# Performance work log

Measured on AMD Instinct MI355X. Metric: run time of the kernel, lower is better.

The kernel has to match this reference:

```python
import jax, jax.numpy as jnp
import numpy as np

B = 4          # documents per batch
L = 128        # unique candidate entity links
S = 2048       # predicted spans (max over batch)
N = 1 + L + S  # root + links + spans


def setup_inputs() -> dict:
    key = jax.random.key(0)
    k1, k2, k3 = jax.random.split(key, 3)
    # coref/linking edge scores over [root | links | spans] x [root | links | spans]
    scores = jax.random.normal(k1, (B, N, N), dtype=jnp.float32) * 0.1
    eye = jnp.eye(N, dtype=jnp.float32)
    # z mask: all admissible edges -- no self loops, no incoming edges to root
    z_mask = jnp.ones((B, N, N), dtype=jnp.float32) * (1.0 - eye)[None]
    z_mask = z_mask.at[:, :, 0].set(0.0)
    # target mask: sparse subset of z edges + root->all so a spanning
    # arborescence always exists (mirrors the gold cluster / gold link edges)
    tgt = (jax.random.uniform(k2, (B, N, N)) < 0.05).astype(jnp.float32) * z_mask
    tgt = tgt.at[:, 0, 1:].set(1.0)
    # ragged valid lengths per batch element (1 + unique_links_len + n_pred_spans)
    lengths = jnp.array([N, N - 256, N - 512, N - 64], dtype=jnp.int32)
    return {"scores": scores, "target_mask": tgt, "z_mask": z_mask, "lengths": lengths}


def _mtt_log_partition(scores, mask, lengths):
    """Matrix-tree theorem log-partition: logdet of the root-minor of the
    Laplacian of exp(scores) restricted to edges in `mask` and to the first
    `lengths[b]` nodes of each batch element."""
    n = scores.shape[-1]
    valid = (jnp.arange(n)[None, :] < lengths[:, None]).astype(scores.dtype)  # [B,N]
    w = jnp.exp(scores) * mask * valid[:, :, None] * valid[:, None, :]        # [B,N,N]
    colsum = jnp.sum(w, axis=-2)                                              # incoming weight per node
    lap = colsum[:, :, None] * jnp.eye(n, dtype=scores.dtype)[None] - w       # L = D_in - W
    minor = lap[:, 1:, 1:]                                                    # drop root row/col
    # pad the diagonal of invalid (past-length) nodes with 1 so they
    # contribute logdet 0 instead of making the minor singular
    pad = 1.0 - valid[:, 1:]
    minor = minor + pad[:, :, None] * jnp.eye(n - 1, dtype=scores.dtype)[None]
    _, logdet = jnp.linalg.slogdet(minor)
    return logdet


def reference(scores, target_mask, z_mask, lengths):
    log_z = _mtt_log_partition(scores, z_mask, lengths)        # log partition over all arborescences
    log_t = _mtt_log_partition(scores, target_mask, lengths)   # log weight of gold arborescences
    return jnp.mean(log_z - log_t)                             # MTT negative log-likelihood
```

## Files before the change

### kernel.cpp

```cpp
#include <hip/hip_runtime.h>
#include <math.h>

#define NFULL 2177
#define NN    2176
#define NB    64
#define NMAT  8
#define NBATCH 4


__global__ void init_cs_kernel(float* __restrict__ cs) {
  int i = blockIdx.x * blockDim.x + threadIdx.x;
  if (i < NMAT * NN) cs[i] = 0.f;
}

__global__ __launch_bounds__(256) void build_fused(const float* __restrict__ scores,
                                                   const float* __restrict__ zm,
                                                   const float* __restrict__ tm,
                                                   const int* __restrict__ lengths,
                                                   float* __restrict__ cs,
                                                   float* __restrict__ M) {
  int c = blockIdx.x * 256 + threadIdx.x;
  if (c >= NN) return;
  int b = blockIdx.z;
  int len = lengths[b];
  int j = c + 1;
  bool jv = (j < len);
  int r0 = blockIdx.y * 64;
  size_t sbase = (size_t)b * NFULL * NFULL + j;
  float az = 0.f, at = 0.f;
  if (blockIdx.y == 0 && jv) {
    float e = __expf(scores[sbase]);
    az += e * zm[sbase];
    at += e * tm[sbase];
  }
  size_t mz = (size_t)b * NN * NN + (size_t)r0 * NN + c;
  size_t mt = (size_t)(NBATCH + b) * NN * NN + (size_t)r0 * NN + c;
  for (int rr = 0; rr < 64; ++rr) {
    int i = r0 + rr + 1;
    float vz = 0.f, vt = 0.f;
    if (jv && i < len) {
      size_t off = sbase + (size_t)i * NFULL;
      float e = __expf(scores[off]);
      vz = e * zm[off];
      vt = e * tm[off];
      az += vz;
      at += vt;
    }
    M[mz] = -vz;
    M[mt] = -vt;
    mz += NN;
    mt += NN;
  }
  if (az != 0.f) atomicAdd(&cs[b * NN + c], az);
  if (at != 0.f) atomicAdd(&cs[(NBATCH + b) * NN + c], at);
}

__global__ void diag_fix(const int* __restrict__ lengths,
                         const float* __restrict__ cs,
                         float* __restrict__ M) {
  int idx = blockIdx.x * 256 + threadIdx.x;
  if (idx >= NMAT * NN) return;
  int mm = idx / NN, c = idx - mm * NN;
  int len = lengths[mm & 3];
  float pad = (c + 1 < len) ? 0.f : 1.f;
  M[(size_t)mm * NN * NN + (size_t)c * NN + c] = cs[idx] + pad;
}


__device__ void factor_invert(float* __restrict__ A,
                              float* __restrict__ invUg,
                              float* __restrict__ invLg,
                              float (*T)[68], float (*X)[68],
                              float* __restrict__ Dinv,
                              int k0, int tid, int do_inv) {
  for (int j = 0; j < 63; ++j) {
    float inv = 1.0f / T[j][j];
    for (int r = j + 1 + tid; r < 64; r += 256) T[r][j] *= inv;
    __syncthreads();
    int rem = 63 - j;
    for (int idx = tid; idx < rem * rem; idx += 256) {
      int rr = j + 1 + idx / rem;
      int cc = j + 1 + idx % rem;
      T[rr][cc] -= T[rr][j] * T[j][cc];
    }
    __syncthreads();
  }
  for (int idx = tid; idx < 64 * 64; idx += 256) {
    int r = idx >> 6, c = idx & 63;
    A[(size_t)(k0 + r) * NN + (k0 + c)] = T[r][c];
  }
  if (!do_inv) return;
  if (tid < 64) Dinv[tid] = 1.0f / T[tid][tid];
  __syncthreads();
  if (tid < 64) {
    int j = tid;
    X[j][j] = Dinv[j];
    for (int i = j - 1; i >= 0; --i) {
      float s = 0.f;
      for (int t = i + 1; t <= j; ++t) s += T[i][t] * X[t][j];
      X[i][j] = -s * Dinv[i];
    }
    for (int i = j + 1; i < 64; ++i) X[i][j] = 0.f;
  }
  __syncthreads();
  for (int idx = tid; idx < 4096; idx += 256) invUg[idx] = X[idx >> 6][idx & 63];
  __syncthreads();
  if (tid < 64) {
    int j = tid;
    X[j][j] = 1.f;
    for (int i = j + 1; i < 64; ++i) {
      float s = 0.f;
      for (int t = j; t < i; ++t) s += T[i][t] * X[t][j];
      X[i][j] = -s;
    }
    for (int i = 0; i < j; ++i) X[i][j] = 0.f;
  }
  __syncthreads();
  for (int idx = tid; idx < 4096; idx += 256) invLg[idx] = X[idx >> 6][idx & 63];
}

__global__ __launch_bounds__(256) void factor0(float* __restrict__ Mb,
                                               float* __restrict__ invUb,
                                               float* __restrict__ invLb) {
  __shared__ float T[64][68];
  __shared__ float X[64][68];
  __shared__ float Dinv[64];
  int m = blockIdx.x, tid = threadIdx.x;
  float* A = Mb + (size_t)m * NN * NN;
  for (int idx = tid; idx < 64 * 64; idx += 256) {
    int r = idx >> 6, c = idx & 63;
    T[r][c] = A[(size_t)r * NN + c];
  }
  __syncthreads();
  factor_invert(A, invUb + (size_t)m * 4096, invLb + (size_t)m * 4096,
                T, X, Dinv, 0, tid, 1);
}

__global__ __launch_bounds__(256) void panel_gemm(float* __restrict__ Mb,
                                                  const float* __restrict__ invUb,
                                                  const float* __restrict__ invLb,
                                                  int k0) {
  __shared__ float Aa[64][68];
  __shared__ float Bb[64][68];
  int m = blockIdx.y, role = blockIdx.z, tid = threadIdx.x;
  float* A = Mb + (size_t)m * NN * NN;
  int obase = k0 + 64 + blockIdx.x * 64;
  if (role == 0) {
    const float* invU = invUb + (size_t)m * 4096;
    for (int idx = tid; idx < 4096; idx += 256) {
      int r = idx >> 6, k = idx & 63;
      Aa[k][r] = A[(size_t)(obase + r) * NN + (k0 + k)];
    }
    for (int idx = tid; idx < 4096; idx += 256)
      Bb[idx >> 6][idx & 63] = invU[idx];
  } else {
    const float* invL = invLb + (size_t)m * 4096;
    for (int idx = tid; idx < 4096; idx += 256) {
      int r = idx >> 6, k = idx & 63;
      Aa[k][r] = invL[(r << 6) + k];
    }
    for (int idx = tid; idx < 4096; idx += 256) {
      int k = idx >> 6, c = idx & 63;
      Bb[k][c] = A[(size_t)(k0 + k) * NN + (obase + c)];
    }
  }
  __syncthreads();
  int c0 = (tid & 15) << 2;
  int r0 = (tid >> 4) << 2;
  float acc[4][4];
#pragma unroll
  for (int i = 0; i < 4; ++i)
#pragma unroll
    for (int jj = 0; jj < 4; ++jj) acc[i][jj] = 0.f;
#pragma unroll 8
  for (int k = 0; k < 64; ++k) {
    float4 a  = *(const float4*)&Aa[k][r0];
    float4 bv = *(const float4*)&Bb[k][c0];
    acc[0][0] += a.x * bv.x; acc[0][1] += a.x * bv.y; acc[0][2] += a.x * bv.z; acc[0][3] += a.x * bv.w;
    acc[1][0] += a.y * bv.x; acc[1][1] += a.y * bv.y; acc[1][2] += a.y * bv.z; acc[1][3] += a.y * bv.w;
    acc[2][0] += a.z * bv.x; acc[2][1] += a.z * bv.y; acc[2][2] += a.z * bv.z; acc[2][3] += a.z * bv.w;
    acc[3][0] += a.w * bv.x; acc[3][1] += a.w * bv.y; acc[3][2] += a.w * bv.z; acc[3][3] += a.w * bv.w;
  }
  if (role == 0) {
#pragma unroll
    for (int i = 0; i < 4; ++i) {
      float4 v = make_float4(acc[i][0], acc[i][1], acc[i][2], acc[i][3]);
      *(float4*)&A[(size_t)(obase + r0 + i) * NN + (k0 + c0)] = v;
    }
  } else {
#pragma unroll
    for (int i = 0; i < 4; ++i) {
      float4 v = make_float4(acc[i][0], acc[i][1], acc[i][2], acc[i][3]);
      *(float4*)&A[(size_t)(k0 + r0 + i) * NN + (obase + c0)] = v;
    }
  }
}

__global__ __launch_bounds__(256) void trail_gemm(float* __restrict__ Mb,
                                                  float* __restrict__ invUb,
                                                  float* __restrict__ invLb,
                                                  int k0, int do_inv) {
  __shared__ float Lt[64][68];
  __shared__ float Ut[64][68];
  __shared__ float Dinv[64];
  int m = blockIdx.z;
  float* A = Mb + (size_t)m * NN * NN;
  int base  = k0 + 64;
  int rbase = base + blockIdx.y * 64;
  int cbase = base + blockIdx.x * 64;
  int tid = threadIdx.x;
  for (int idx = tid; idx < 64 * 64; idx += 256) {
    int r = idx >> 6, k = idx & 63;
    Lt[k][r] = A[(size_t)(rbase + r) * NN + (k0 + k)];
  }
  for (int idx = tid; idx < 64 * 64; idx += 256) {
    int k = idx >> 6, c = idx & 63;
    Ut[k][c] = A[(size_t)(k0 + k) * NN + (cbase + c)];
  }
  __syncthreads();
  int c0 = (tid & 15) << 2;
  int r0 = (tid >> 4) << 2;
  float acc[4][4];
#pragma unroll
  for (int i = 0; i < 4; ++i)
#pragma unroll
    for (int jj = 0; jj < 4; ++jj) acc[i][jj] = 0.f;
#pragma unroll 8
  for (int k = 0; k < 64; ++k) {
    float4 a  = *(const float4*)&Lt[k][r0];
    float4 bv = *(const float4*)&Ut[k][c0];
    acc[0][0] += a.x * bv.x; acc[0][1] += a.x * bv.y; acc[0][2] += a.x * bv.z; acc[0][3] += a.x * bv.w;
    acc[1][0] += a.y * bv.x; acc[1][1] += a.y * bv.y; acc[1][2] += a.y * bv.z; acc[1][3] += a.y * bv.w;
    acc[2][0] += a.z * bv.x; acc[2][1] += a.z * bv.y; acc[2][2] += a.z * bv.z; acc[2][3] += a.z * bv.w;
    acc[3][0] += a.w * bv.x; acc[3][1] += a.w * bv.y; acc[3][2] += a.w * bv.z; acc[3][3] += a.w * bv.w;
  }
  bool special = (blockIdx.x == 0 && blockIdx.y == 0);
  if (!special) {
#pragma unroll
    for (int i = 0; i < 4; ++i) {
      float4* p = (float4*)&A[(size_t)(rbase + r0 + i) * NN + (cbase + c0)];
      float4 v = *p;
      v.x -= acc[i][0]; v.y -= acc[i][1]; v.z -= acc[i][2]; v.w -= acc[i][3];
      *p = v;
    }
    return;
  }
  __syncthreads();
#pragma unroll
  for (int i = 0; i < 4; ++i) {
    const float4* p = (const float4*)&A[(size_t)(rbase + r0 + i) * NN + (cbase + c0)];
    float4 v = *p;
    v.x -= acc[i][0]; v.y -= acc[i][1]; v.z -= acc[i][2]; v.w -= acc[i][3];
    *(float4*)&Lt[r0 + i][c0] = v;
  }
  __syncthreads();
  factor_invert(A, invUb + (size_t)m * 4096, invLb + (size_t)m * 4096,
                Lt, Ut, Dinv, base, tid, do_inv);
}


__global__ void logdet_kernel(const float* __restrict__ Mb, double* __restrict__ dlog) {
  int m = blockIdx.x;
  const float* A = Mb + (size_t)m * NN * NN;
  double s = 0.0;
  for (int i = threadIdx.x; i < NN; i += 256)
    s += (double)logf(fabsf(A[(size_t)i * NN + i]));
  __shared__ double red[256];
  red[threadIdx.x] = s;
  __syncthreads();
  for (int k = 128; k > 0; k >>= 1) {
    if (threadIdx.x < k) red[threadIdx.x] += red[threadIdx.x + k];
    __syncthreads();
  }
  if (threadIdx.x == 0) dlog[m] = red[0];
}

__global__ void final_kernel(const double* __restrict__ dlog, float* __restrict__ out) {
  if (threadIdx.x == 0) {
    double acc = 0.0;
    for (int b = 0; b < NBATCH; ++b) acc += dlog[b] - dlog[NBATCH + b];
    out[0] = (float)(acc * 0.25);
  }
}


extern "C" void kernel_launch(void* const* d_in, const int* in_sizes, int n_in,
                              void* d_out, int out_size, void* d_ws, size_t ws_size,
                              hipStream_t stream) {
  const float* scores  = (const float*)d_in[0];
  const float* tm      = (const float*)d_in[1];
  const float* zm      = (const float*)d_in[2];
  const int*   lengths = (const int*)d_in[3];
  float* out = (float*)d_out;

  float* M  = (float*)d_ws;
  float* cs = M + (size_t)NMAT * NN * NN;
  double* dlog = (double*)(cs + (size_t)NMAT * NN);
  float* invU = (float*)(dlog + NMAT);
  float* invL = invU + (size_t)NMAT * 4096;

  init_cs_kernel<<<(NMAT * NN + 255) / 256, 256, 0, stream>>>(cs);
  build_fused<<<dim3((NN + 255) / 256, NN / 64, NBATCH), 256, 0, stream>>>(
      scores, zm, tm, lengths, cs, M);
  diag_fix<<<(NMAT * NN + 255) / 256, 256, 0, stream>>>(lengths, cs, M);
  factor0<<<NMAT, 256, 0, stream>>>(M, invU, invL);

  for (int k0 = 0; k0 + NB < NN; k0 += NB) {
    int rem = NN - k0 - NB;
    panel_gemm<<<dim3(rem / 64, NMAT, 2), 256, 0, stream>>>(M, invU, invL, k0);
    trail_gemm<<<dim3(rem / 64, rem / 64, NMAT), 256, 0, stream>>>(
        M, invU, invL, k0, rem > 64 ? 1 : 0);
  }

  logdet_kernel<<<NMAT, 256, 0, stream>>>(M, dlog);
  final_kernel<<<1, 64, 0, stream>>>(dlog, out);
}
```

Measured before the change: 5.321 ms.

## Use 128x128 trailing-update tiles and restructure diagonal block factorization

Result: slower. 5.774 ms (+8.5%).

```diff
diff --git a/kernel.cpp b/kernel.cpp
--- a/kernel.cpp
+++ b/kernel.cpp
@@ -6,6 +6,10 @@
 #define NB    64
 #define NMAT  8
 #define NBATCH 4
+#define TP    65
+#define LTP   132
+#define UTP   140
+#define SSZ   8704
 
 
 __global__ void init_cs_kernel(float* __restrict__ cs) {
@@ -67,73 +71,55 @@
 }
 
 
-__device__ void factor_invert(float* __restrict__ A,
-                              float* __restrict__ invUg,
-                              float* __restrict__ invLg,
-                              float (*T)[68], float (*X)[68],
-                              float* __restrict__ Dinv,
-                              int k0, int tid, int do_inv) {
+__device__ __forceinline__ void factor64(float* T, int tid) {
+  int c = tid & 63, g = tid >> 6;
   for (int j = 0; j < 63; ++j) {
-    float inv = 1.0f / T[j][j];
-    for (int r = j + 1 + tid; r < 64; r += 256) T[r][j] *= inv;
+    float inv = 1.0f / T[j * TP + j];
+    int rs = j + 1 + ((g - j - 1) & 3);
+    if (c == j) {
+      for (int r = rs; r < 64; r += 4) T[r * TP + j] *= inv;
+    }
     __syncthreads();
-    int rem = 63 - j;
-    for (int idx = tid; idx < rem * rem; idx += 256) {
-      int rr = j + 1 + idx / rem;
-      int cc = j + 1 + idx % rem;
-      T[rr][cc] -= T[rr][j] * T[j][cc];
+    if (c > j) {
+      float ujc = T[j * TP + c];
+      for (int r = rs; r < 64; r += 4) T[r * TP + c] -= T[r * TP + j] * ujc;
     }
     __syncthreads();
   }
-  for (int idx = tid; idx < 64 * 64; idx += 256) {
-    int r = idx >> 6, c = idx & 63;
-    A[(size_t)(k0 + r) * NN + (k0 + c)] = T[r][c];
-  }
-  if (!do_inv) return;
-  if (tid < 64) Dinv[tid] = 1.0f / T[tid][tid];
-  __syncthreads();
-  if (tid < 64) {
-    int j = tid;
-    X[j][j] = Dinv[j];
-    for (int i = j - 1; i >= 0; --i) {
-      float s = 0.f;
-      for (int t = i + 1; t <= j; ++t) s += T[i][t] * X[t][j];
-      X[i][j] = -s * Dinv[i];
-    }
-    for (int i = j + 1; i < 64; ++i) X[i][j] = 0.f;
-  }
-  __syncthreads();
-  for (int idx = tid; idx < 4096; idx += 256) invUg[idx] = X[idx >> 6][idx & 63];
-  __syncthreads();
-  if (tid < 64) {
-    int j = tid;
-    X[j][j] = 1.f;
-    for (int i = j + 1; i < 64; ++i) {
-      float s = 0.f;
-      for (int t = j; t < i; ++t) s += T[i][t] * X[t][j];
-      X[i][j] = -s;
-    }
-    for (int i = 0; i < j; ++i) X[i][j] = 0.f;
-  }
-  __syncthreads();
-  for (int idx = tid; idx < 4096; idx += 256) invLg[idx] = X[idx >> 6][idx & 63];
-}
-
-__global__ __launch_bounds__(256) void factor0(float* __restrict__ Mb,
-                                               float* __restrict__ invUb,
-                                               float* __restrict__ invLb) {
-  __shared__ float T[64][68];
-  __shared__ float X[64][68];
-  __shared__ float Dinv[64];
+}
+
+__device__ __forceinline__ void invertUL(const float* T, float* X,
+                                         float* __restrict__ invUg,
+                                         float* __restrict__ invLg, int tid) {
+  if (tid >= 64) return;
+  int j = tid;
+  for (int i = 63; i >= 0; --i) {
+    float s = (j == i) ? 1.f : 0.f;
+    for (int t = i + 1; t < 64; ++t) s -= T[i * TP + t] * X[t * TP + j];
+    X[i * TP + j] = s / T[i * TP + i];
+  }
+  for (int i = 0; i < 64; ++i) invUg[i * 64 + j] = X[i * TP + j];
+  for (int i = 0; i < 64; ++i) {
+    float s = (j == i) ? 1.f : 0.f;
+    for (int t = 0; t < i; ++t) s -= T[i * TP + t] * X[t * TP + j];
+    X[i * TP + j] = s;
+  }
+  for (int i = 0; i < 64; ++i) invLg[i * 64 + j] = X[i * TP + j];
+}
+
+__global__ __launch_bounds__(256, 2) void factor0(float* __restrict__ Mb,
+                                                  float* __restrict__ invUb,
+                                                  float* __restrict__ invLb) {
+  __shared__ float S[SSZ];
   int m = blockIdx.x, tid = threadIdx.x;
   float* A = Mb + (size_t)m * NN * NN;
-  for (int idx = tid; idx < 64 * 64; idx += 256) {
-    int r = idx >> 6, c = idx & 63;
-    T[r][c] = A[(size_t)r * NN + c];
-  }
-  __syncthreads();
-  factor_invert(A, invUb + (size_t)m * 4096, invLb + (size_t)m * 4096,
-                T, X, Dinv, 0, tid, 1);
+  for (int idx = tid; idx < 4096; idx += 256)
+    S[(idx >> 6) * TP + (idx & 63)] = A[(size_t)(idx >> 6) * NN + (idx & 63)];
+  __syncthreads();
+  factor64(S, tid);
+  for (int idx = tid; idx < 4096; idx += 256)
+    A[(size_t)(idx >> 6) * NN + (idx & 63)] = S[(idx >> 6) * TP + (idx & 63)];
+  invertUL(S, S + 4480, invUb + (size_t)m * 4096, invLb + (size_t)m * 4096, tid);
 }
 
 __global__ __launch_bounds__(256) void panel_gemm(float* __restrict__ Mb,
@@ -196,66 +182,106 @@
   }
 }
 
-__global__ __launch_bounds__(256) void trail_gemm(float* __restrict__ Mb,
-                                                  float* __restrict__ invUb,
-                                                  float* __restrict__ invLb,
-                                                  int k0, int do_inv) {
-  __shared__ float Lt[64][68];
-  __shared__ float Ut[64][68];
-  __shared__ float Dinv[64];
-  int m = blockIdx.z;
+__global__ __launch_bounds__(256, 2) void trail_gemm(float* __restrict__ Mb,
+                                                     float* __restrict__ invUb,
+                                                     float* __restrict__ invLb,
+                                                     int k0, int do_inv) {
+  __shared__ float S[SSZ];
+  int m = blockIdx.x;
+  int txt = blockIdx.y, tyt = blockIdx.z;
   float* A = Mb + (size_t)m * NN * NN;
-  int base  = k0 + 64;
-  int rbase = base + blockIdx.y * 64;
-  int cbase = base + blockIdx.x * 64;
+  int base = k0 + NB;
+  int rem  = NN - base;
+  int rbase = base + tyt * 128, cbase = base + txt * 128;
+  int rows = rem - tyt * 128; if (rows > 128) rows = 128;
+  int cols = rem - txt * 128; if (cols > 128) cols = 128;
   int tid = threadIdx.x;
-  for (int idx = tid; idx < 64 * 64; idx += 256) {
-    int r = idx >> 6, k = idx & 63;
-    Lt[k][r] = A[(size_t)(rbase + r) * NN + (k0 + k)];
-  }
-  for (int idx = tid; idx < 64 * 64; idx += 256) {
-    int k = idx >> 6, c = idx & 63;
-    Ut[k][c] = A[(size_t)(k0 + k) * NN + (cbase + c)];
-  }
-  __syncthreads();
-  int c0 = (tid & 15) << 2;
-  int r0 = (tid >> 4) << 2;
-  float acc[4][4];
-#pragma unroll
-  for (int i = 0; i < 4; ++i)
-#pragma unroll
-    for (int jj = 0; jj < 4; ++jj) acc[i][jj] = 0.f;
+  int tx = tid & 15, ty = tid >> 4;
+  int rr = ty * 8, cc = tx * 8;
+  int cs0 = cc + ((cc >> 5) << 2);
+  float acc[8][8];
+#pragma unroll
+  for (int i = 0; i < 8; ++i)
+#pragma unroll
+    for (int j = 0; j < 8; ++j) acc[i][j] = 0.f;
+
+  for (int h = 0; h < 2; ++h) {
+    if (h) __syncthreads();
+    int kb = k0 + h * 32;
+    for (int idx = tid; idx < 4096; idx += 256) {
+      int k = idx & 31, r = idx >> 5;
+      int gr = rbase + (r < rows ? r : 0);
+      S[k * LTP + r] = A[(size_t)gr * NN + kb + k];
+    }
+    for (int idx = tid; idx < 4096; idx += 256) {
+      int c = idx & 127, k = idx >> 7;
+      int gc = cbase + (c < cols ? c : 0);
+      S[4224 + k * UTP + c + ((c >> 5) << 2)] = A[(size_t)(kb + k) * NN + gc];
+    }
+    __syncthreads();
 #pragma unroll 8
-  for (int k = 0; k < 64; ++k) {
-    float4 a  = *(const float4*)&Lt[k][r0];
-    float4 bv = *(const float4*)&Ut[k][c0];
-    acc[0][0] += a.x * bv.x; acc[0][1] += a.x * bv.y; acc[0][2] += a.x * bv.z; acc[0][3] += a.x * bv.w;
-    acc[1][0] += a.y * bv.x; acc[1][1] += a.y * bv.y; acc[1][2] += a.y * bv.z; acc[1][3] += a.y * bv.w;
-    acc[2][0] += a.z * bv.x; acc[2][1] += a.z * bv.y; acc[2][2] += a.z * bv.z; acc[2][3] += a.z * bv.w;
-    acc[3][0] += a.w * bv.x; acc[3][1] += a.w * bv.y; acc[3][2] += a.w * bv.z; acc[3][3] += a.w * bv.w;
-  }
-  bool special = (blockIdx.x == 0 && blockIdx.y == 0);
+    for (int k = 0; k < 32; ++k) {
+      const float* lp = &S[k * LTP + rr];
+      const float* up = &S[4224 + k * UTP + cs0];
+      float4 a0 = *(const float4*)lp;
+      float4 a1 = *(const float4*)(lp + 4);
+      float4 b0 = *(const float4*)up;
+      float4 b1 = *(const float4*)(up + 4);
+      float af[8] = {a0.x, a0.y, a0.z, a0.w, a1.x, a1.y, a1.z, a1.w};
+      float bf[8] = {b0.x, b0.y, b0.z, b0.w, b1.x, b1.y, b1.z, b1.w};
+#pragma unroll
+      for (int i = 0; i < 8; ++i)
+#pragma unroll
+        for (int j = 0; j < 8; ++j) acc[i][j] += af[i] * bf[j];
+    }
+  }
+
+  bool special = (txt == 0 && tyt == 0);
   if (!special) {
-#pragma unroll
-    for (int i = 0; i < 4; ++i) {
-      float4* p = (float4*)&A[(size_t)(rbase + r0 + i) * NN + (cbase + c0)];
-      float4 v = *p;
-      v.x -= acc[i][0]; v.y -= acc[i][1]; v.z -= acc[i][2]; v.w -= acc[i][3];
-      *p = v;
+    if (cc < cols) {
+#pragma unroll
+      for (int i = 0; i < 8; ++i) {
+        int r = rr + i;
+        if (r < rows) {
+          float4* p = (float4*)&A[(size_t)(rbase + r) * NN + cbase + cc];
+          float4 v0 = p[0], v1 = p[1];
+          v0.x -= acc[i][0]; v0.y -= acc[i][1]; v0.z -= acc[i][2]; v0.w -= acc[i][3];
+          v1.x -= acc[i][4]; v1.y -= acc[i][5]; v1.z -= acc[i][6]; v1.w -= acc[i][7];
+          p[0] = v0; p[1] = v1;
+        }
+      }
     }
     return;
   }
   __syncthreads();
-#pragma unroll
-  for (int i = 0; i < 4; ++i) {
-    const float4* p = (const float4*)&A[(size_t)(rbase + r0 + i) * NN + (cbase + c0)];
-    float4 v = *p;
-    v.x -= acc[i][0]; v.y -= acc[i][1]; v.z -= acc[i][2]; v.w -= acc[i][3];
-    *(float4*)&Lt[r0 + i][c0] = v;
-  }
-  __syncthreads();
-  factor_invert(A, invUb + (size_t)m * 4096, invLb + (size_t)m * 4096,
-                Lt, Ut, Dinv, base, tid, do_inv);
+  float* T = S;
+  if (cc < cols) {
+#pragma unroll
+    for (int i = 0; i < 8; ++i) {
+      int r = rr + i;
+      if (r < rows) {
+        float4* p = (float4*)&A[(size_t)(rbase + r) * NN + cbase + cc];
+        float4 v0 = p[0], v1 = p[1];
+        v0.x -= acc[i][0]; v0.y -= acc[i][1]; v0.z -= acc[i][2]; v0.w -= acc[i][3];
+        v1.x -= acc[i][4]; v1.y -= acc[i][5]; v1.z -= acc[i][6]; v1.w -= acc[i][7];
+        if (r < 64 && cc < 64) {
+          float* t = &T[r * TP + cc];
+          t[0] = v0.x; t[1] = v0.y; t[2] = v0.z; t[3] = v0.w;
+          t[4] = v1.x; t[5] = v1.y; t[6] = v1.z; t[7] = v1.w;
+        } else {
+          p[0] = v0; p[1] = v1;
+        }
+      }
+    }
+  }
+  __syncthreads();
+  factor64(T, tid);
+  for (int idx = tid; idx < 4096; idx += 256) {
+    int r = idx >> 6, c = idx & 63;
+    A[(size_t)(base + r) * NN + base + c] = T[r * TP + c];
+  }
+  if (do_inv)
+    invertUL(T, S + 4480, invUb + (size_t)m * 4096, invLb + (size_t)m * 4096, tid);
 }
 
 
@@ -308,7 +334,8 @@
   for (int k0 = 0; k0 + NB < NN; k0 += NB) {
     int rem = NN - k0 - NB;
     panel_gemm<<<dim3(rem / 64, NMAT, 2), 256, 0, stream>>>(M, invU, invL, k0);
-    trail_gemm<<<dim3(rem / 64, rem / 64, NMAT), 256, 0, stream>>>(
+    int nt = (rem + 127) / 128;
+    trail_gemm<<<dim3(NMAT, nt, nt), 256, 0, stream>>>(
         M, invU, invL, k0, rem > 64 ? 1 : 0);
   }
 
```
